# Kernel optimization log

Hardware: AMD Instinct MI355X
Metric: run time of the kernel (lower is better)

## Reference

```python
import jax, jax.numpy as jnp
import numpy as np


def setup_inputs() -> dict:
    key = jax.random.key(0)
    k1, k2, k3 = jax.random.split(key, 3)
    B, T, D, H = 256, 100, 4096, 1024
    # Xavier-uniform style init scales for the two parameter matrices
    zlim = float(np.sqrt(6.0 / (H + D)))
    klim = float(np.sqrt(6.0 / (D + H)))
    x = (jax.random.uniform(k1, (B, T, D), dtype=jnp.float32) < 0.1).astype(jnp.float32)  # sparse basket indicators
    Z = jax.random.uniform(k2, (H, D), dtype=jnp.float32, minval=-zlim, maxval=zlim)
    KFinv = jax.random.uniform(k3, (D, H), dtype=jnp.float32, minval=-klim, maxval=klim)
    b_out = jnp.zeros((D,), dtype=jnp.float32)
    b_hidden = jnp.zeros((H,), dtype=jnp.float32)
    return {"x": x, "Z": Z, "b_out": b_out, "KFinv": KFinv, "b_hidden": b_hidden}


def reference(x, Z, b_out, KFinv, b_hidden):
    # x: [B, T, D]; Z: [H, D]; KFinv: [D, H]
    B = x.shape[0]
    H = Z.shape[0]
    # initial hidden state is zeros -> initial next_basket = b_out (no sigmoid on step 0 prediction)
    h0 = jnp.zeros((H,), dtype=x.dtype)
    nb0 = jnp.broadcast_to(h0 @ Z + b_out, (B, Z.shape[1]))  # [B, D]

    def step(next_basket, xt):
        # xt: [B, D]
        diff = xt - next_basket                      # [B, D]
        hidden = diff @ KFinv + b_hidden             # [B, H]
        nb = jax.nn.sigmoid(hidden @ Z + b_out)      # [B, D]
        return nb, nb

    xs = jnp.swapaxes(x, 0, 1)                       # [T, B, D]
    _, preds = jax.lax.scan(step, nb0, xs)           # preds: [T, B, D]
    return jnp.swapaxes(preds, 0, 1)                 # [B, T, D]
```

## Files before the change

### kernel.cpp

```cpp
#include <hip/hip_runtime.h>
#include <hip/hip_cooperative_groups.h>

#define T_SEQ 100
#define DD 4096
#define HH 1024
#define BB 256

#define GRID_WG 256
#define BLOCK_T 512

typedef __attribute__((ext_vector_type(8))) short short8;
typedef __attribute__((ext_vector_type(4))) float float4_t;

__device__ __forceinline__ short f2bf(float f) {
  union { float f; unsigned u; } v; v.f = f;
  unsigned r = v.u + 0x7fffu + ((v.u >> 16) & 1u);
  return (short)(r >> 16);
}

__device__ __forceinline__ int swz(int row, int col) {
  return col ^ ((row & 7) << 3);
}

__global__ __launch_bounds__(256) void transpose_cvt(const float* __restrict__ src,
                                                     short* __restrict__ dst,
                                                     int K, int N) {
  __shared__ float tile[32][33];
  int k0 = blockIdx.x * 32, n0 = blockIdx.y * 32;
  int tx = threadIdx.x & 31, ty = threadIdx.x >> 5;
#pragma unroll
  for (int i = 0; i < 32; i += 8)
    tile[ty + i][tx] = src[(size_t)(k0 + ty + i) * N + n0 + tx];
  __syncthreads();
#pragma unroll
  for (int i = 0; i < 32; i += 8)
    dst[(size_t)(n0 + ty + i) * K + k0 + tx] = f2bf(tile[tx][ty + i]);
}

__global__ __launch_bounds__(BLOCK_T, 2) void gru_persist(
    const float* __restrict__ x, const short* __restrict__ KFt ,
    const short* __restrict__ Zt , const float* __restrict__ b_out,
    const float* __restrict__ b_hidden, short* __restrict__ diff ,
    short* __restrict__ hb , float* __restrict__ out) {
  __shared__ short smem[2][2][8192];
  auto grid = cooperative_groups::this_grid();

  const int g = blockIdx.x, tid = threadIdx.x;
  const int lane = tid & 63, wid = tid >> 6;
  const int quad = lane >> 4, l15 = lane & 15;
  const int gsize = GRID_WG * BLOCK_T;
  const int gtid = g * BLOCK_T + tid;

  for (int idx = gtid; idx < BB * DD / 2; idx += gsize) {
    int m = idx >> 11, d = (idx & 2047) * 2;
    const float* xp = &x[(size_t)m * T_SEQ * DD + d];
    unsigned lo = (unsigned short)f2bf(xp[0] - b_out[d]);
    unsigned hi = (unsigned short)f2bf(xp[1] - b_out[d + 1]);
    ((unsigned*)diff)[idx] = lo | (hi << 16);
  }

  const int xcd = g & 7, loc = g >> 3;
  const int maA = (loc & 7) * 32;
  const int naA = (4 * xcd + (loc >> 3)) * 32;
  const int wkA = wid >> 2, wqA = wid & 3;
  const int wmA = wqA >> 1, wnA = wqA & 1;
  const int maB = (loc & 3) * 64;
  const int naB = (8 * xcd + (loc >> 2)) * 64;
  const int wmB = wid >> 1, wnB = wid & 1;
  const int srA = tid >> 4, scA = tid & 15;
  const int srB = tid >> 3, scB = tid & 7;

  short8 wK[2], wD[2], wZ[2], wH[2];

#pragma unroll
  for (int j = 0; j < 2; ++j)
    wK[j] = *(const short8*)&KFt[(size_t)(naA + srA) * DD + scA * 8 + j * 128];

  grid.sync();

  for (int t = 0; t < T_SEQ; ++t) {
    {
      float4_t acc = {0.f, 0.f, 0.f, 0.f};
#pragma unroll
      for (int j = 0; j < 2; ++j)
        wD[j] = *(const short8*)&diff[(size_t)(maA + srA) * DD + scA * 8 + j * 128];
#pragma unroll
      for (int j = 0; j < 2; ++j) {
        int co = swz(srA, scA * 8 + j * 128);
        *(short8*)&smem[0][0][srA * 256 + co] = wD[j];
        *(short8*)&smem[0][1][srA * 256 + co] = wK[j];
      }
      int cur = 0;
      const int arow = wmA * 16 + l15, brow = wnA * 16 + l15;
      const int ko = wkA * 128;
#pragma unroll 1
      for (int it = 0; it < 16; ++it) {
        __syncthreads();
        if (it < 15) {
          const int kb = (it + 1) * 256;
#pragma unroll
          for (int j = 0; j < 2; ++j) {
            wD[j] = *(const short8*)&diff[(size_t)(maA + srA) * DD + kb + scA * 8 + j * 128];
            wK[j] = *(const short8*)&KFt[(size_t)(naA + srA) * DD + kb + scA * 8 + j * 128];
          }
        }
        const short* sA = smem[cur][0];
        const short* sB = smem[cur][1];
#pragma unroll
        for (int ks = 0; ks < 4; ++ks) {
          short8 a = *(const short8*)&sA[arow * 256 + swz(arow, ko + ks * 32 + quad * 8)];
          short8 b = *(const short8*)&sB[brow * 256 + swz(brow, ko + ks * 32 + quad * 8)];
          acc = __builtin_amdgcn_mfma_f32_16x16x32_bf16(a, b, acc, 0, 0, 0);
        }
        if (it < 15) {
          cur ^= 1;
#pragma unroll
          for (int j = 0; j < 2; ++j) {
            int co = swz(srA, scA * 8 + j * 128);
            *(short8*)&smem[cur][0][srA * 256 + co] = wD[j];
            *(short8*)&smem[cur][1][srA * 256 + co] = wK[j];
          }
        }
      }
      __syncthreads();
      float* red = (float*)&smem[0][0][0];
      if (wkA == 1) {
#pragma unroll
        for (int r = 0; r < 4; ++r) red[(wqA * 64 + lane) * 4 + r] = acc[r];
      }
      __syncthreads();
      if (wkA == 0) {
#pragma unroll
        for (int r = 0; r < 4; ++r) {
          float v = acc[r] + red[(wqA * 64 + lane) * 4 + r];
          int m = maA + wmA * 16 + quad * 4 + r;
          int n = naA + wnA * 16 + l15;
          float hv = v + b_hidden[n];
          float ov = __shfl_xor(hv, 1);
          if (!(lane & 1)) {
            unsigned w = (unsigned)(unsigned short)f2bf(hv) |
                         ((unsigned)(unsigned short)f2bf(ov) << 16);
            *(unsigned*)&hb[m * HH + n] = w;
          }
        }
      }
    }
#pragma unroll
    for (int j = 0; j < 2; ++j)
      wZ[j] = *(const short8*)&Zt[(size_t)(naB + srB) * HH + scB * 8 + j * 64];
    grid.sync();

    {
      float4_t acc2[2] = {};
      float xr[8];
      if (t < T_SEQ - 1) {
#pragma unroll
        for (int f = 0; f < 2; ++f)
#pragma unroll
          for (int r = 0; r < 4; ++r) {
            int m = maB + wmB * 16 + quad * 4 + r;
            int n = naB + wnB * 32 + f * 16 + l15;
            xr[f * 4 + r] = x[((size_t)m * T_SEQ + t + 1) * DD + n];
          }
      }
#pragma unroll
      for (int j = 0; j < 2; ++j)
        wH[j] = *(const short8*)&hb[(size_t)(maB + srB) * HH + scB * 8 + j * 64];
#pragma unroll
      for (int j = 0; j < 2; ++j) {
        int co = swz(srB, scB * 8 + j * 64);
        *(short8*)&smem[0][0][srB * 128 + co] = wH[j];
        *(short8*)&smem[0][1][srB * 128 + co] = wZ[j];
      }
      int cur = 0;
      const int arowB = wmB * 16 + l15;
      const int b0row = wnB * 32 + l15, b1row = wnB * 32 + 16 + l15;
#pragma unroll 1
      for (int it = 0; it < 8; ++it) {
        __syncthreads();
        if (it < 7) {
          const int kb = (it + 1) * 128;
#pragma unroll
          for (int j = 0; j < 2; ++j) {
            wH[j] = *(const short8*)&hb[(size_t)(maB + srB) * HH + kb + scB * 8 + j * 64];
            wZ[j] = *(const short8*)&Zt[(size_t)(naB + srB) * HH + kb + scB * 8 + j * 64];
          }
        }
        const short* sA = smem[cur][0];
        const short* sB = smem[cur][1];
#pragma unroll
        for (int ks = 0; ks < 4; ++ks) {
          short8 a  = *(const short8*)&sA[arowB * 128 + swz(arowB, ks * 32 + quad * 8)];
          short8 b0 = *(const short8*)&sB[b0row * 128 + swz(b0row, ks * 32 + quad * 8)];
          short8 b1 = *(const short8*)&sB[b1row * 128 + swz(b1row, ks * 32 + quad * 8)];
          acc2[0] = __builtin_amdgcn_mfma_f32_16x16x32_bf16(a, b0, acc2[0], 0, 0, 0);
          acc2[1] = __builtin_amdgcn_mfma_f32_16x16x32_bf16(a, b1, acc2[1], 0, 0, 0);
        }
        if (it < 7) {
          cur ^= 1;
#pragma unroll
          for (int j = 0; j < 2; ++j) {
            int co = swz(srB, scB * 8 + j * 64);
            *(short8*)&smem[cur][0][srB * 128 + co] = wH[j];
            *(short8*)&smem[cur][1][srB * 128 + co] = wZ[j];
          }
        }
      }
#pragma unroll
      for (int f = 0; f < 2; ++f)
#pragma unroll
        for (int r = 0; r < 4; ++r) {
          int m = maB + wmB * 16 + quad * 4 + r;
          int n = naB + wnB * 32 + f * 16 + l15;
          float z = acc2[f][r] + b_out[n];
          float s = 1.f / (1.f + __expf(-z));
          out[((size_t)m * T_SEQ + t) * DD + n] = s;
          if (t < T_SEQ - 1) {
            short db = f2bf(xr[f * 4 + r] - s);
            int ob = __shfl_xor((int)(unsigned short)db, 1);
            if (!(lane & 1)) {
              unsigned w = (unsigned)(unsigned short)db | ((unsigned)ob << 16);
              *(unsigned*)&diff[(size_t)m * DD + n] = w;
            }
          }
        }
    }
    if (t < T_SEQ - 1) {
#pragma unroll
      for (int j = 0; j < 2; ++j)
        wK[j] = *(const short8*)&KFt[(size_t)(naA + srA) * DD + scA * 8 + j * 128];
    }
    grid.sync();
  }
}

extern "C" void kernel_launch(void* const* d_in, const int* in_sizes, int n_in,
                              void* d_out, int out_size, void* d_ws, size_t ws_size,
                              hipStream_t stream) {
  const float* x = (const float*)d_in[0];
  const float* Z = (const float*)d_in[1];
  const float* b_out = (const float*)d_in[2];
  const float* KFinv = (const float*)d_in[3];
  const float* b_hidden = (const float*)d_in[4];
  float* out = (float*)d_out;

  char* ws = (char*)d_ws;
  short* KFt = (short*)ws;
  short* Zt = (short*)(ws + 8388608);
  short* diff = (short*)(ws + 16777216);
  short* hb = (short*)(ws + 18874368);

  transpose_cvt<<<dim3(128, 32), 256, 0, stream>>>(KFinv, KFt, 4096, 1024);
  transpose_cvt<<<dim3(32, 128), 256, 0, stream>>>(Z, Zt, 1024, 4096);

  void* args[] = {(void*)&x,        (void*)&KFt,  (void*)&Zt, (void*)&b_out,
                  (void*)&b_hidden, (void*)&diff, (void*)&hb, (void*)&out};
  hipLaunchCooperativeKernel((void*)gru_persist, dim3(GRID_WG), dim3(BLOCK_T), args, 0,
                             stream);
}
```

Measured before the change: 8.666 ms.

## Load MFMA operands directly from global memory into registers, dropping LDS staging

Both GEMM phases now load A and B fragments straight from global/L2 into registers in MFMA operand layout, double-buffering in registers, instead of staging tiles through swizzled shared memory with __syncthreads per k-step. This removes LDS round trips and block barriers inside the inner loops, and LDS is cut to a small reduction buffer. Launch bounds drop to one block per SM, allowing more registers for the larger register buffers. The cost is less coalesced global loads (each lane reads 16-byte pieces from separate rows) and the loss of the early KFt/Z prefetch before the grid syncs.

```diff
diff --git a/kernel.cpp b/kernel.cpp
--- a/kernel.cpp
+++ b/kernel.cpp
@@ -16,10 +16,6 @@
   union { float f; unsigned u; } v; v.f = f;
   unsigned r = v.u + 0x7fffu + ((v.u >> 16) & 1u);
   return (short)(r >> 16);
-}
-
-__device__ __forceinline__ int swz(int row, int col) {
-  return col ^ ((row & 7) << 3);
 }
 
 __global__ __launch_bounds__(256) void transpose_cvt(const float* __restrict__ src,
@@ -37,12 +33,12 @@
     dst[(size_t)(n0 + ty + i) * K + k0 + tx] = f2bf(tile[tx][ty + i]);
 }
 
-__global__ __launch_bounds__(BLOCK_T, 2) void gru_persist(
+__global__ __launch_bounds__(BLOCK_T, 1) void gru_persist(
     const float* __restrict__ x, const short* __restrict__ KFt ,
     const short* __restrict__ Zt , const float* __restrict__ b_out,
     const float* __restrict__ b_hidden, short* __restrict__ diff ,
     short* __restrict__ hb , float* __restrict__ out) {
-  __shared__ short smem[2][2][8192];
+  __shared__ float red[1024];
   auto grid = cooperative_groups::this_grid();
 
   const int g = blockIdx.x, tid = threadIdx.x;
@@ -67,63 +63,43 @@
   const int maB = (loc & 3) * 64;
   const int naB = (8 * xcd + (loc >> 2)) * 64;
   const int wmB = wid >> 1, wnB = wid & 1;
-  const int srA = tid >> 4, scA = tid & 15;
-  const int srB = tid >> 3, scB = tid & 7;
-
-  short8 wK[2], wD[2], wZ[2], wH[2];
-
-#pragma unroll
-  for (int j = 0; j < 2; ++j)
-    wK[j] = *(const short8*)&KFt[(size_t)(naA + srA) * DD + scA * 8 + j * 128];
 
   grid.sync();
 
   for (int t = 0; t < T_SEQ; ++t) {
     {
+      const int ar = maA + wmA * 16 + l15;
+      const int br = naA + wnA * 16 + l15;
+      const short* pa = diff + (size_t)ar * DD + wkA * 2048 + quad * 8;
+      const short* pb = KFt + (size_t)br * DD + wkA * 2048 + quad * 8;
       float4_t acc = {0.f, 0.f, 0.f, 0.f};
-#pragma unroll
-      for (int j = 0; j < 2; ++j)
-        wD[j] = *(const short8*)&diff[(size_t)(maA + srA) * DD + scA * 8 + j * 128];
-#pragma unroll
-      for (int j = 0; j < 2; ++j) {
-        int co = swz(srA, scA * 8 + j * 128);
-        *(short8*)&smem[0][0][srA * 256 + co] = wD[j];
-        *(short8*)&smem[0][1][srA * 256 + co] = wK[j];
-      }
-      int cur = 0;
-      const int arow = wmA * 16 + l15, brow = wnA * 16 + l15;
-      const int ko = wkA * 128;
+      short8 a0[8], b0[8], a1[8], b1[8];
+#pragma unroll
+      for (int j = 0; j < 8; ++j) {
+        a0[j] = *(const short8*)(pa + j * 32);
+        b0[j] = *(const short8*)(pb + j * 32);
+      }
 #pragma unroll 1
-      for (int it = 0; it < 16; ++it) {
-        __syncthreads();
-        if (it < 15) {
-          const int kb = (it + 1) * 256;
-#pragma unroll
-          for (int j = 0; j < 2; ++j) {
-            wD[j] = *(const short8*)&diff[(size_t)(maA + srA) * DD + kb + scA * 8 + j * 128];
-            wK[j] = *(const short8*)&KFt[(size_t)(naA + srA) * DD + kb + scA * 8 + j * 128];
-          }
-        }
-        const short* sA = smem[cur][0];
-        const short* sB = smem[cur][1];
-#pragma unroll
-        for (int ks = 0; ks < 4; ++ks) {
-          short8 a = *(const short8*)&sA[arow * 256 + swz(arow, ko + ks * 32 + quad * 8)];
-          short8 b = *(const short8*)&sB[brow * 256 + swz(brow, ko + ks * 32 + quad * 8)];
-          acc = __builtin_amdgcn_mfma_f32_16x16x32_bf16(a, b, acc, 0, 0, 0);
-        }
-        if (it < 15) {
-          cur ^= 1;
-#pragma unroll
-          for (int j = 0; j < 2; ++j) {
-            int co = swz(srA, scA * 8 + j * 128);
-            *(short8*)&smem[cur][0][srA * 256 + co] = wD[j];
-            *(short8*)&smem[cur][1][srA * 256 + co] = wK[j];
-          }
-        }
-      }
-      __syncthreads();
-      float* red = (float*)&smem[0][0][0];
+      for (int kb = 0; kb < 2048; kb += 512) {
+#pragma unroll
+        for (int j = 0; j < 8; ++j) {
+          a1[j] = *(const short8*)(pa + kb + 256 + j * 32);
+          b1[j] = *(const short8*)(pb + kb + 256 + j * 32);
+        }
+#pragma unroll
+        for (int j = 0; j < 8; ++j)
+          acc = __builtin_amdgcn_mfma_f32_16x16x32_bf16(a0[j], b0[j], acc, 0, 0, 0);
+        if (kb + 512 < 2048) {
+#pragma unroll
+          for (int j = 0; j < 8; ++j) {
+            a0[j] = *(const short8*)(pa + kb + 512 + j * 32);
+            b0[j] = *(const short8*)(pb + kb + 512 + j * 32);
+          }
+        }
+#pragma unroll
+        for (int j = 0; j < 8; ++j)
+          acc = __builtin_amdgcn_mfma_f32_16x16x32_bf16(a1[j], b1[j], acc, 0, 0, 0);
+      }
       if (wkA == 1) {
 #pragma unroll
         for (int r = 0; r < 4; ++r) red[(wqA * 64 + lane) * 4 + r] = acc[r];
@@ -145,9 +121,6 @@
         }
       }
     }
-#pragma unroll
-    for (int j = 0; j < 2; ++j)
-      wZ[j] = *(const short8*)&Zt[(size_t)(naB + srB) * HH + scB * 8 + j * 64];
     grid.sync();
 
     {
@@ -163,47 +136,43 @@
             xr[f * 4 + r] = x[((size_t)m * T_SEQ + t + 1) * DD + n];
           }
       }
-#pragma unroll
-      for (int j = 0; j < 2; ++j)
-        wH[j] = *(const short8*)&hb[(size_t)(maB + srB) * HH + scB * 8 + j * 64];
-#pragma unroll
-      for (int j = 0; j < 2; ++j) {
-        int co = swz(srB, scB * 8 + j * 64);
-        *(short8*)&smem[0][0][srB * 128 + co] = wH[j];
-        *(short8*)&smem[0][1][srB * 128 + co] = wZ[j];
-      }
-      int cur = 0;
-      const int arowB = wmB * 16 + l15;
-      const int b0row = wnB * 32 + l15, b1row = wnB * 32 + 16 + l15;
+      const int am = maB + wmB * 16 + l15;
+      const int bn = naB + wnB * 32 + l15;
+      const short* ph = hb + (size_t)am * HH + quad * 8;
+      const short* pz0 = Zt + (size_t)bn * HH + quad * 8;
+      const short* pz1 = pz0 + (size_t)16 * HH;
+      short8 h0[4], u0[4], v0[4], h1[4], u1[4], v1[4];
+#pragma unroll
+      for (int j = 0; j < 4; ++j) {
+        h0[j] = *(const short8*)(ph + j * 32);
+        u0[j] = *(const short8*)(pz0 + j * 32);
+        v0[j] = *(const short8*)(pz1 + j * 32);
+      }
 #pragma unroll 1
-      for (int it = 0; it < 8; ++it) {
-        __syncthreads();
-        if (it < 7) {
-          const int kb = (it + 1) * 128;
-#pragma unroll
-          for (int j = 0; j < 2; ++j) {
-            wH[j] = *(const short8*)&hb[(size_t)(maB + srB) * HH + kb + scB * 8 + j * 64];
-            wZ[j] = *(const short8*)&Zt[(size_t)(naB + srB) * HH + kb + scB * 8 + j * 64];
-          }
-        }
-        const short* sA = smem[cur][0];
-        const short* sB = smem[cur][1];
-#pragma unroll
-        for (int ks = 0; ks < 4; ++ks) {
-          short8 a  = *(const short8*)&sA[arowB * 128 + swz(arowB, ks * 32 + quad * 8)];
-          short8 b0 = *(const short8*)&sB[b0row * 128 + swz(b0row, ks * 32 + quad * 8)];
-          short8 b1 = *(const short8*)&sB[b1row * 128 + swz(b1row, ks * 32 + quad * 8)];
-          acc2[0] = __builtin_amdgcn_mfma_f32_16x16x32_bf16(a, b0, acc2[0], 0, 0, 0);
-          acc2[1] = __builtin_amdgcn_mfma_f32_16x16x32_bf16(a, b1, acc2[1], 0, 0, 0);
-        }
-        if (it < 7) {
-          cur ^= 1;
-#pragma unroll
-          for (int j = 0; j < 2; ++j) {
-            int co = swz(srB, scB * 8 + j * 64);
-            *(short8*)&smem[cur][0][srB * 128 + co] = wH[j];
-            *(short8*)&smem[cur][1][srB * 128 + co] = wZ[j];
-          }
+      for (int kb = 0; kb < 1024; kb += 256) {
+#pragma unroll
+        for (int j = 0; j < 4; ++j) {
+          h1[j] = *(const short8*)(ph + kb + 128 + j * 32);
+          u1[j] = *(const short8*)(pz0 + kb + 128 + j * 32);
+          v1[j] = *(const short8*)(pz1 + kb + 128 + j * 32);
+        }
+#pragma unroll
+        for (int j = 0; j < 4; ++j) {
+          acc2[0] = __builtin_amdgcn_mfma_f32_16x16x32_bf16(h0[j], u0[j], acc2[0], 0, 0, 0);
+          acc2[1] = __builtin_amdgcn_mfma_f32_16x16x32_bf16(h0[j], v0[j], acc2[1], 0, 0, 0);
+        }
+        if (kb + 256 < 1024) {
+#pragma unroll
+          for (int j = 0; j < 4; ++j) {
+            h0[j] = *(const short8*)(ph + kb + 256 + j * 32);
+            u0[j] = *(const short8*)(pz0 + kb + 256 + j * 32);
+            v0[j] = *(const short8*)(pz1 + kb + 256 + j * 32);
+          }
+        }
+#pragma unroll
+        for (int j = 0; j < 4; ++j) {
+          acc2[0] = __builtin_amdgcn_mfma_f32_16x16x32_bf16(h1[j], u1[j], acc2[0], 0, 0, 0);
+          acc2[1] = __builtin_amdgcn_mfma_f32_16x16x32_bf16(h1[j], v1[j], acc2[1], 0, 0, 0);
         }
       }
 #pragma unroll
@@ -225,11 +194,6 @@
           }
         }
     }
-    if (t < T_SEQ - 1) {
-#pragma unroll
-      for (int j = 0; j < 2; ++j)
-        wK[j] = *(const short8*)&KFt[(size_t)(naA + srA) * DD + scA * 8 + j * 128];
-    }
     grid.sync();
   }
 }
```

After: 11.30 ms. 30.4% more time.
